# Kernel tuning notes

Measured on AMD Instinct MI355X. Metric: run time of the kernel, lower is better.

Reference implementation:

```python
import jax, jax.numpy as jnp
import numpy as np

jax.config.update("jax_enable_x64", True)


def setup_inputs() -> dict:
    H = 131072          # num_hints
    N = 1_048_576       # number of DB entries (rows of `entries`)
    BLOCK = 1024        # block_size; blocks and offsets both in [0, BLOCK)
    MAXSZ = 128         # per-hint subset size in [1, MAXSZ)
    rng = np.random.default_rng(0)

    sizes = rng.integers(1, MAXSZ, size=H)               # ragged segment sizes
    starts = np.concatenate([[0], np.cumsum(sizes)[:-1]])  # CSR exclusive prefix
    T = int(sizes.sum())                                  # ~8.4M total indices

    blocks = rng.integers(0, BLOCK, size=T)
    offsets = rng.integers(0, BLOCK, size=T)
    entries = rng.integers(0, 2**62, size=(N, 5), dtype=np.int64)

    return {
        "entries": jnp.asarray(entries, dtype=jnp.int64),
        "subset_blocks": jnp.asarray(blocks, dtype=jnp.int64),
        "subset_offsets": jnp.asarray(offsets, dtype=jnp.int64),
        "subset_starts": jnp.asarray(starts, dtype=jnp.int64),
        "subset_sizes": jnp.asarray(sizes, dtype=jnp.int64),
        "block_size": BLOCK,
    }


def reference(entries, subset_blocks, subset_offsets, subset_starts, subset_sizes, block_size):
    """Gather + variable-length segment XOR reduction.

    entries:        [N, 5] int64
    subset_blocks:  [T]    int64 flat ragged buffer
    subset_offsets: [T]    int64 flat ragged buffer
    subset_starts:  [H]    int64 CSR-style start of each hint's slice
    subset_sizes:   [H]    int64 length of each hint's slice
    returns:        [H, 5] int64 XOR parities (zeros for empty hints)
    """
    n = entries.shape[0]
    idx = jnp.clip(subset_blocks * block_size + subset_offsets, 0, n - 1)  # [T]
    selected = entries[idx]                                                # [T, 5]

    # Prefix-XOR along the flat token axis; XOR is associative so
    # segment XOR = cum[start+size] ^ cum[start] with cum[0] = 0.
    cum = jax.lax.associative_scan(jnp.bitwise_xor, selected, axis=0)      # [T, 5]
    cum = jnp.concatenate([jnp.zeros((1, 5), dtype=entries.dtype), cum], axis=0)

    ends = subset_starts + subset_sizes
    parities = jnp.bitwise_xor(cum[ends], cum[subset_starts])              # [H, 5]
    return parities
```

## Files before the change

kernel.cpp:

```cpp
#include <hip/hip_runtime.h>


#define HPG        128
#define NSL        16
#define STAGE_CAP  12288

__device__ __forceinline__ int clip_idx(int v, int N) {
    return min(max(v, 0), N - 1);
}

__global__ __launch_bounds__(1024) void bucket_kernel(
    const int* __restrict__ blocks,
    const int* __restrict__ offsets,
    const int* __restrict__ starts,
    const int* __restrict__ bs_ptr,
    const int* __restrict__ entries,
    int* __restrict__ out,
    unsigned int* __restrict__ buck,
    unsigned int* __restrict__ tab,
    int H, int N, int T)
{
    __shared__ unsigned int stage[STAGE_CAP];
    __shared__ int lstart[HPG + 1];
    __shared__ unsigned int cnt[NSL], off[NSL], lcur[NSL];

    const int g  = blockIdx.x;
    const int t  = threadIdx.x;
    const int h0 = g * HPG;
    const int h1 = min(H, h0 + HPG);
    const int nh = h1 - h0;
    const int bs = bs_ptr[0];

    if (t < nh) lstart[t] = starts[h0 + t];
    if (t == 0) lstart[nh] = (h1 < H) ? starts[h1] : T;
    if (t < NSL) { cnt[t] = 0; lcur[t] = 0; }
    __syncthreads();

    const int tokBase = lstart[0];
    const int count   = lstart[nh] - tokBase;
    const int staged  = min(count, STAGE_CAP);

    for (int i = t; i < staged; i += 1024) {
        const int gpos = tokBase + i;
        const int idx  = clip_idx(blocks[gpos] * bs + offsets[gpos], N);
        int lo = 0, hi = nh - 1;
        while (lo < hi) {
            int m = (lo + hi + 1) >> 1;
            if (lstart[m] <= gpos) lo = m; else hi = m - 1;
        }
        stage[i] = (unsigned int)idx | ((unsigned int)lo << 20);
        atomicAdd(&cnt[(unsigned int)idx >> 16], 1u);
    }
    __syncthreads();

    if (t == 0) {
        unsigned int run = 0;
        for (int s = 0; s < NSL; ++s) { off[s] = run; run += cnt[s]; }
    }
    __syncthreads();

    if (t < NSL) {
        tab[(g * NSL + t) * 2 + 0] = (unsigned int)tokBase + off[t];
        tab[(g * NSL + t) * 2 + 1] = cnt[t];
    }

    for (int i = t; i < staged; i += 1024) {
        const unsigned int w = stage[i];
        const unsigned int s = (w >> 16) & (NSL - 1);
        const unsigned int r = atomicAdd(&lcur[s], 1u);
        buck[(unsigned int)tokBase + off[s] + r] = w;
    }

    for (int i = staged + t; i < count; i += 1024) {
        const int gpos = tokBase + i;
        const int idx  = clip_idx(blocks[gpos] * bs + offsets[gpos], N);
        int lo = 0, hi = nh - 1;
        while (lo < hi) {
            int m = (lo + hi + 1) >> 1;
            if (lstart[m] <= gpos) lo = m; else hi = m - 1;
        }
        const int* row = entries + (long)idx * 5;
        int* o5 = out + (long)(h0 + lo) * 5;
        atomicXor(&o5[0], row[0]); atomicXor(&o5[1], row[1]);
        atomicXor(&o5[2], row[2]); atomicXor(&o5[3], row[3]);
        atomicXor(&o5[4], row[4]);
    }
}

__global__ __launch_bounds__(256) void gather_kernel(
    const unsigned int* __restrict__ buck,
    const unsigned int* __restrict__ tab,
    const int* __restrict__ entries,
    int* __restrict__ out,
    int H, int NG, int nSl, int groupsPerBlock)
{
    __shared__ int acc[HPG * 5];

    const int B = blockIdx.x;
    const int x = B & 7;
    const int g0 = B >> 3;
    const int t = threadIdx.x;
    const int gStride = gridDim.x >> 3;

    for (int k = 0; k < groupsPerBlock; ++k) {
        const int g = g0 + k * gStride;
        if (g >= NG) break;

        for (int i = t; i < HPG * 5; i += 256) acc[i] = 0;
        __syncthreads();

        for (int s = x; s < nSl; s += 8) {
            const unsigned int base = tab[(g * NSL + s) * 2 + 0];
            const unsigned int cn   = tab[(g * NSL + s) * 2 + 1];

            unsigned int i = t;
            for (; i + 256 < cn; i += 512) {
                const unsigned int w0 = buck[base + i];
                const unsigned int w1 = buck[base + i + 256];
                const int idx0 = (int)(w0 & 0xFFFFFu);
                const int idx1 = (int)(w1 & 0xFFFFFu);
                const int h0   = (int)(w0 >> 20);
                const int h1   = (int)(w1 >> 20);
                const int* r0 = entries + (long)idx0 * 5;
                const int* r1 = entries + (long)idx1 * 5;
                const int a0 = r0[0], a1 = r0[1], a2 = r0[2], a3 = r0[3], a4 = r0[4];
                const int b0 = r1[0], b1 = r1[1], b2 = r1[2], b3 = r1[3], b4 = r1[4];
                atomicXor(&acc[h0 * 5 + 0], a0);
                atomicXor(&acc[h0 * 5 + 1], a1);
                atomicXor(&acc[h0 * 5 + 2], a2);
                atomicXor(&acc[h0 * 5 + 3], a3);
                atomicXor(&acc[h0 * 5 + 4], a4);
                atomicXor(&acc[h1 * 5 + 0], b0);
                atomicXor(&acc[h1 * 5 + 1], b1);
                atomicXor(&acc[h1 * 5 + 2], b2);
                atomicXor(&acc[h1 * 5 + 3], b3);
                atomicXor(&acc[h1 * 5 + 4], b4);
            }
            if (i < cn) {
                const unsigned int w = buck[base + i];
                const int idx = (int)(w & 0xFFFFFu);
                const int h   = (int)(w >> 20);
                const int* row = entries + (long)idx * 5;
                atomicXor(&acc[h * 5 + 0], row[0]);
                atomicXor(&acc[h * 5 + 1], row[1]);
                atomicXor(&acc[h * 5 + 2], row[2]);
                atomicXor(&acc[h * 5 + 3], row[3]);
                atomicXor(&acc[h * 5 + 4], row[4]);
            }
        }
        __syncthreads();

        const long obase = (long)g * HPG * 5;
        const long omax  = (long)H * 5;
        for (int i = t; i < HPG * 5; i += 256) {
            const long o = obase + i;
            if (o < omax) {
                const int v = acc[i];
                if (v) atomicXor(&out[o], v);
            }
        }
        __syncthreads();
    }
}

__global__ __launch_bounds__(256) void hint_xor_wave(
    const int* __restrict__ entries,
    const int* __restrict__ blocks,
    const int* __restrict__ offsets,
    const int* __restrict__ starts,
    const int* __restrict__ sizes,
    const int* __restrict__ bs_ptr,
    int* __restrict__ out,
    int H, int N)
{
    const int gtid = blockIdx.x * blockDim.x + threadIdx.x;
    const int hint = gtid >> 6;
    const int lane = gtid & 63;
    if (hint >= H) return;

    const int start = starts[hint];
    const int size  = sizes[hint];
    const int bs    = bs_ptr[0];

    int a0 = 0, a1 = 0, a2 = 0, a3 = 0, a4 = 0;
    for (int j = lane; j < size; j += 64) {
        int idx = clip_idx(blocks[start + j] * bs + offsets[start + j], N);
        const int* row = entries + (size_t)idx * 5;
        a0 ^= row[0]; a1 ^= row[1]; a2 ^= row[2]; a3 ^= row[3]; a4 ^= row[4];
    }
    #pragma unroll
    for (int m = 1; m < 64; m <<= 1) {
        a0 ^= __shfl_xor(a0, m);
        a1 ^= __shfl_xor(a1, m);
        a2 ^= __shfl_xor(a2, m);
        a3 ^= __shfl_xor(a3, m);
        a4 ^= __shfl_xor(a4, m);
    }
    if (lane == 0) {
        int* o = out + (size_t)hint * 5;
        o[0] = a0; o[1] = a1; o[2] = a2; o[3] = a3; o[4] = a4;
    }
}

extern "C" void kernel_launch(void* const* d_in, const int* in_sizes, int n_in,
                              void* d_out, int out_size, void* d_ws, size_t ws_size,
                              hipStream_t stream) {
    const int* entries = (const int*)d_in[0];
    const int* blocks  = (const int*)d_in[1];
    const int* offsets = (const int*)d_in[2];
    const int* starts  = (const int*)d_in[3];
    const int* sizes   = (const int*)d_in[4];
    const int* bs      = (const int*)d_in[5];
    int* out = (int*)d_out;

    const int H = in_sizes[3];
    const int T = in_sizes[1];
    const int N = in_sizes[0] / 5;

    const int NG  = (H + HPG - 1) / HPG;
    const int nSl = (N + 65535) >> 16;

    const size_t buckOff   = 0;
    const size_t buckBytes = (size_t)T * 4;
    const size_t tabOff    = (buckOff + buckBytes + 63) & ~(size_t)63;
    const size_t need      = tabOff + (size_t)NG * NSL * 2 * 4 + 64;

    const bool ok = (N <= (1 << 20)) && (nSl <= NSL) && (ws_size >= need) &&
                    (H <= (1 << 27));

    if (ok) {
        unsigned int* buck = (unsigned int*)((char*)d_ws + buckOff);
        unsigned int* tab  = (unsigned int*)((char*)d_ws + tabOff);

        hipMemsetAsync(d_out, 0, (size_t)out_size * sizeof(int), stream);

        hipLaunchKernelGGL(bucket_kernel, dim3(NG), dim3(1024), 0, stream,
                           blocks, offsets, starts, bs, entries, out,
                           buck, tab, H, N, T);

        int gridB = 2048;
        if (gridB > NG * 8) gridB = NG * 8;
        const int gStride = (gridB >= 8) ? (gridB >> 3) : 1;
        const int gpb = (NG + gStride - 1) / gStride;

        hipLaunchKernelGGL(gather_kernel, dim3(gridB), dim3(256), 0, stream,
                           buck, tab, entries, out, H, NG, nSl, gpb);
    } else {
        const long total_threads = (long)H * 64;
        const int block = 256;
        const int grid = (int)((total_threads + block - 1) / block);
        hipLaunchKernelGGL(hint_xor_wave, dim3(grid), dim3(block), 0, stream,
                           entries, blocks, offsets, starts, sizes, bs, out, H, N);
    }
}
```

Baseline: 189.1 us.

## Bucket tokens into fixed-capacity per-slice slots in one pass, fold memset into kernel

The bucket kernel now scatters each token straight into a fixed-capacity slot region per (group, slice) using a shared atomic cursor. This drops the LDS staging array, the count/prefix pass and the second scatter pass. Tokens beyond the 768-entry capacity fall back to global atomic XOR into the output. The output zeroing moves from a separate hipMemsetAsync into the bucket kernel, at the cost of a larger, sparsely filled bucket workspace.

```diff
diff --git a/kernel.cpp b/kernel.cpp
--- a/kernel.cpp
+++ b/kernel.cpp
@@ -1,9 +1,9 @@
 #include <hip/hip_runtime.h>
 
 
-#define HPG        128
-#define NSL        16
-#define STAGE_CAP  12288
+#define HPG   128
+#define NSL   16
+#define CAP   768
 
 __device__ __forceinline__ int clip_idx(int v, int N) {
     return min(max(v, 0), N - 1);
@@ -17,12 +17,11 @@
     const int* __restrict__ entries,
     int* __restrict__ out,
     unsigned int* __restrict__ buck,
-    unsigned int* __restrict__ tab,
+    unsigned int* __restrict__ tabCnt,
     int H, int N, int T)
 {
-    __shared__ unsigned int stage[STAGE_CAP];
     __shared__ int lstart[HPG + 1];
-    __shared__ unsigned int cnt[NSL], off[NSL], lcur[NSL];
+    __shared__ unsigned int lcur[NSL];
 
     const int g  = blockIdx.x;
     const int t  = threadIdx.x;
@@ -33,14 +32,19 @@
 
     if (t < nh) lstart[t] = starts[h0 + t];
     if (t == 0) lstart[nh] = (h1 < H) ? starts[h1] : T;
-    if (t < NSL) { cnt[t] = 0; lcur[t] = 0; }
+    if (t < NSL) lcur[t] = 0;
+
+    {
+        const long obase = (long)h0 * 5;
+        const long ocnt  = (long)nh * 5;
+        for (long i = t; i < ocnt; i += 1024) out[obase + i] = 0;
+    }
     __syncthreads();
 
     const int tokBase = lstart[0];
     const int count   = lstart[nh] - tokBase;
-    const int staged  = min(count, STAGE_CAP);
-
-    for (int i = t; i < staged; i += 1024) {
+
+    for (int i = t; i < count; i += 1024) {
         const int gpos = tokBase + i;
         const int idx  = clip_idx(blocks[gpos] * bs + offsets[gpos], N);
         int lo = 0, hi = nh - 1;
@@ -48,48 +52,27 @@
             int m = (lo + hi + 1) >> 1;
             if (lstart[m] <= gpos) lo = m; else hi = m - 1;
         }
-        stage[i] = (unsigned int)idx | ((unsigned int)lo << 20);
-        atomicAdd(&cnt[(unsigned int)idx >> 16], 1u);
+        const unsigned int s = (unsigned int)idx >> 16;
+        const unsigned int r = atomicAdd(&lcur[s], 1u);
+        if (r < CAP) {
+            buck[((size_t)(g * NSL) + s) * CAP + r] =
+                (unsigned int)idx | ((unsigned int)lo << 20);
+        } else {
+            const int* row = entries + (long)idx * 5;
+            int* o5 = out + (long)(h0 + lo) * 5;
+            atomicXor(&o5[0], row[0]); atomicXor(&o5[1], row[1]);
+            atomicXor(&o5[2], row[2]); atomicXor(&o5[3], row[3]);
+            atomicXor(&o5[4], row[4]);
+        }
     }
     __syncthreads();
 
-    if (t == 0) {
-        unsigned int run = 0;
-        for (int s = 0; s < NSL; ++s) { off[s] = run; run += cnt[s]; }
-    }
-    __syncthreads();
-
-    if (t < NSL) {
-        tab[(g * NSL + t) * 2 + 0] = (unsigned int)tokBase + off[t];
-        tab[(g * NSL + t) * 2 + 1] = cnt[t];
-    }
-
-    for (int i = t; i < staged; i += 1024) {
-        const unsigned int w = stage[i];
-        const unsigned int s = (w >> 16) & (NSL - 1);
-        const unsigned int r = atomicAdd(&lcur[s], 1u);
-        buck[(unsigned int)tokBase + off[s] + r] = w;
-    }
-
-    for (int i = staged + t; i < count; i += 1024) {
-        const int gpos = tokBase + i;
-        const int idx  = clip_idx(blocks[gpos] * bs + offsets[gpos], N);
-        int lo = 0, hi = nh - 1;
-        while (lo < hi) {
-            int m = (lo + hi + 1) >> 1;
-            if (lstart[m] <= gpos) lo = m; else hi = m - 1;
-        }
-        const int* row = entries + (long)idx * 5;
-        int* o5 = out + (long)(h0 + lo) * 5;
-        atomicXor(&o5[0], row[0]); atomicXor(&o5[1], row[1]);
-        atomicXor(&o5[2], row[2]); atomicXor(&o5[3], row[3]);
-        atomicXor(&o5[4], row[4]);
-    }
+    if (t < NSL) tabCnt[g * NSL + t] = min(lcur[t], (unsigned int)CAP);
 }
 
 __global__ __launch_bounds__(256) void gather_kernel(
     const unsigned int* __restrict__ buck,
-    const unsigned int* __restrict__ tab,
+    const unsigned int* __restrict__ tabCnt,
     const int* __restrict__ entries,
     int* __restrict__ out,
     int H, int NG, int nSl, int groupsPerBlock)
@@ -110,8 +93,8 @@
         __syncthreads();
 
         for (int s = x; s < nSl; s += 8) {
-            const unsigned int base = tab[(g * NSL + s) * 2 + 0];
-            const unsigned int cn   = tab[(g * NSL + s) * 2 + 1];
+            const size_t base = ((size_t)(g * NSL) + s) * CAP;
+            const unsigned int cn = tabCnt[g * NSL + s];
 
             unsigned int i = t;
             for (; i + 256 < cn; i += 512) {
@@ -221,22 +204,20 @@
     const int nSl = (N + 65535) >> 16;
 
     const size_t buckOff   = 0;
-    const size_t buckBytes = (size_t)T * 4;
+    const size_t buckBytes = (size_t)NG * NSL * CAP * 4;
     const size_t tabOff    = (buckOff + buckBytes + 63) & ~(size_t)63;
-    const size_t need      = tabOff + (size_t)NG * NSL * 2 * 4 + 64;
+    const size_t need      = tabOff + (size_t)NG * NSL * 4 + 64;
 
     const bool ok = (N <= (1 << 20)) && (nSl <= NSL) && (ws_size >= need) &&
                     (H <= (1 << 27));
 
     if (ok) {
-        unsigned int* buck = (unsigned int*)((char*)d_ws + buckOff);
-        unsigned int* tab  = (unsigned int*)((char*)d_ws + tabOff);
-
-        hipMemsetAsync(d_out, 0, (size_t)out_size * sizeof(int), stream);
+        unsigned int* buck   = (unsigned int*)((char*)d_ws + buckOff);
+        unsigned int* tabCnt = (unsigned int*)((char*)d_ws + tabOff);
 
         hipLaunchKernelGGL(bucket_kernel, dim3(NG), dim3(1024), 0, stream,
                            blocks, offsets, starts, bs, entries, out,
-                           buck, tab, H, N, T);
+                           buck, tabCnt, H, N, T);
 
         int gridB = 2048;
         if (gridB > NG * 8) gridB = NG * 8;
@@ -244,7 +225,7 @@
         const int gpb = (NG + gStride - 1) / gStride;
 
         hipLaunchKernelGGL(gather_kernel, dim3(gridB), dim3(256), 0, stream,
-                           buck, tab, entries, out, H, NG, nSl, gpb);
+                           buck, tabCnt, entries, out, H, NG, nSl, gpb);
     } else {
         const long total_threads = (long)H * 64;
         const int block = 256;
```

New measurement: 196.9 us. 4.1% more time.
